# Performance work log

Hardware: AMD Instinct MI355X
Metric: run time of the kernel (lower is better)

Reference implementation:

```python
import jax, jax.numpy as jnp
import numpy as np

FP, DP, K, S, B, T, H, ZD = 96, 28, 3, 4, 64, 8, 512, 2
CP = FP - DP + 1          # 69, valid cross-correlation output size
NP = CP * CP              # 4761 = num_pixels


def setup_inputs() -> dict:
    key = jax.random.key(0)
    ks = jax.random.split(key, 12)
    def rn(k, shape, s=0.02):
        return jax.random.normal(k, shape, jnp.float32) * s
    return {
        "frames": jax.random.uniform(ks[0], (S, B, T, FP, FP), jnp.float32),
        "conv_kernel": jax.random.uniform(ks[1], (S, B, K, DP, DP), jnp.float32),
        "eps": jax.random.normal(ks[2], (S, B, K, ZD), jnp.float32),
        "W1": rn(ks[3], (NP, H)), "b1": jnp.zeros((H,), jnp.float32),
        "Wm1": rn(ks[4], (H, H // 2)), "bm1": jnp.zeros((H // 2,), jnp.float32),
        "Wm2": rn(ks[5], (H // 2, ZD)), "bm2": jnp.zeros((ZD,), jnp.float32),
        "Ws1": rn(ks[6], (H, H // 2)), "bs1": jnp.zeros((H // 2,), jnp.float32),
        "Ws2": rn(ks[7], (H // 2, ZD)), "bs2": jnp.zeros((ZD,), jnp.float32),
        "timestep": 0,
    }


def _axis_weights(p, n):
    """Bilinear 1-D gather indices/weights with zero padding outside [0, n)."""
    p0 = jnp.floor(p)
    f = p - p0
    i0 = p0.astype(jnp.int32)
    i1 = i0 + 1
    w0 = jnp.where((i0 >= 0) & (i0 < n), 1.0 - f, 0.0)
    w1 = jnp.where((i1 >= 0) & (i1 < n), f, 0.0)
    return jnp.clip(i0, 0, n - 1), jnp.clip(i1, 0, n - 1), w0, w1


def _place_digit(digit, zw):
    """AT.digit_to_frame: place DPxDP digit into FPxFP frame at z_where (torch
    affine_grid/grid_sample, align_corners=False, zero padding). theta scale =
    FP/DP, translation = -z_where*FP/DP, i.e. in_coord = (FP/DP)*(out - zw)."""
    scale = FP / DP
    out_c = (2.0 * jnp.arange(FP, dtype=jnp.float32) + 1.0) / FP - 1.0  # (FP,)
    px = ((scale * (out_c - zw[0]) + 1.0) * DP - 1.0) * 0.5  # x source pix
    py = ((scale * (out_c - zw[1]) + 1.0) * DP - 1.0) * 0.5  # y source pix
    y0, y1, wy0, wy1 = _axis_weights(py, DP)
    x0, x1, wx0, wx1 = _axis_weights(px, DP)
    # separable bilinear: interp rows then cols
    tmp = wy0[:, None] * digit[y0, :] + wy1[:, None] * digit[y1, :]  # (FP,DP)
    return wx0[None, :] * tmp[:, x0] + wx1[None, :] * tmp[:, x1]     # (FP,FP)

_place_batch = jax.vmap(_place_digit)


def reference(frames, conv_kernel, eps, W1, b1, Wm1, bm1, Wm2, bm2,
              Ws1, bs1, Ws2, bs2, timestep):
    SB = S * B
    frame_left = frames[:, :, timestep]  # (S,B,FP,FP)
    means, stds, zs = [], [], []
    for k in range(K):
        # per-sample dynamic-kernel cross-correlation via grouped conv
        lhs = frame_left.reshape(1, SB, FP, FP)
        rhs = conv_kernel[:, :, k].reshape(SB, 1, DP, DP)
        conved = jax.lax.conv_general_dilated(
            lhs, rhs, (1, 1), 'VALID', feature_group_count=SB)  # (1,SB,CP,CP)
        scores = jax.nn.softmax(conved.reshape(S, B, NP), axis=-1)
        h = jax.nn.relu(scores @ W1 + b1)                       # (S,B,H)
        mean_k = jnp.tanh(jax.nn.relu(h @ Wm1 + bm1) @ Wm2 + bm2)
        std_k = jnp.exp(jax.nn.relu(h @ Ws1 + bs1) @ Ws2 + bs2)
        z_k = mean_k + std_k * eps[:, :, k]                     # rsample
        recon = _place_batch(conv_kernel[:, :, k].reshape(SB, DP, DP),
                             z_k.reshape(SB, ZD)).reshape(S, B, FP, FP)
        frame_left = frame_left - recon
        means.append(mean_k); stds.append(std_k); zs.append(z_k)
    q_mean = jnp.stack(means, 2)    # (S,B,K,2)
    q_std = jnp.stack(stds, 2)
    z_where = jnp.stack(zs, 2)
    return jnp.stack([q_mean, q_std, z_where], 0)  # (3,S,B,K,2)
```

## Files before the change

### kernel.cpp

```cpp
#include <hip/hip_runtime.h>
#include <hip/hip_bf16.h>
#include <math.h>

#define FPD 96
#define DPD 28
#define CPD 69
#define NPD 4761
#define KKC 3
#define SBN 256
#define TT 8
#define HD 512
#define ZDD 2
#define KPAD 4768
#define SPLITK 15
#define FRS 100

typedef __attribute__((ext_vector_type(8))) short bf16x8;
typedef __attribute__((ext_vector_type(4))) float f32x4;

__device__ __forceinline__ float bf2f(ushort u) {
    union { unsigned int i; float f; } v; v.i = ((unsigned int)u) << 16; return v.f;
}

__global__ __launch_bounds__(256) void w1t_kernel(
    const float* __restrict__ W1, ushort* __restrict__ W1T)
{
    __shared__ ushort tile[64][65];
    const int k0 = blockIdx.x * 64;
    const int n0 = blockIdx.y * 64;
    const int t = threadIdx.x;
    const int ln = t & 63;
    const int lr = t >> 6;

    #pragma unroll
    for (int i = 0; i < 16; ++i) {
        int kk = k0 + lr + i * 4;
        float v = (kk < NPD) ? W1[(size_t)kk * HD + n0 + ln] : 0.f;
        __hip_bfloat16 h = __float2bfloat16(v);
        tile[lr + i * 4][ln] = *reinterpret_cast<ushort*>(&h);
    }
    __syncthreads();
    #pragma unroll
    for (int i = 0; i < 16; ++i) {
        int nn = lr + i * 4;
        int kk = k0 + ln;
        if (kk < KPAD)
            W1T[(size_t)(n0 + nn) * KPAD + kk] = tile[ln][nn];
    }
}

__global__ __launch_bounds__(256) void whid_kernel(
    const float* __restrict__ Wm1, const float* __restrict__ Ws1,
    ushort* __restrict__ Whid)
{
    int i = blockIdx.x * 256 + threadIdx.x;
    const float* src = (i >= 131072) ? Ws1 : Wm1;
    float v = src[i & 131071];
    __hip_bfloat16 h = __float2bfloat16(v);
    Whid[i] = *reinterpret_cast<ushort*>(&h);
}

__global__ __launch_bounds__(1024) void conv_softmax_kernel(
    const float* __restrict__ frames, const int* __restrict__ tsp,
    float* __restrict__ frameL, const float* __restrict__ ck,
    const float* __restrict__ z_cur,
    ushort* __restrict__ e_buf, float* __restrict__ inv_denom, int k)
{
    __shared__ __align__(16) float fr[96 * FRS];
    __shared__ __align__(16) float kr[784];
    __shared__ float dg[784];
    __shared__ float cv[4][NPD];
    __shared__ float red[32];

    const int t = threadIdx.x;
    const int ib = blockIdx.x;

    if (t < 784) {
        kr[t] = ck[((size_t)ib * KKC + k) * 784 + t];
        if (k > 0) dg[t] = ck[((size_t)ib * KKC + (k - 1)) * 784 + t];
    }
    float zx = 0.f, zy = 0.f;
    if (k > 0) { zx = z_cur[ib * 2]; zy = z_cur[ib * 2 + 1]; }
    __syncthreads();

    const float* src = (k < 2)
        ? frames + ((size_t)ib * TT + *tsp) * 9216
        : frameL + (size_t)ib * 9216;
    const float scale = 96.f / 28.f;
    for (int p = t; p < 9216; p += 1024) {
        int r = p / 96, c = p - r * 96;
        float val = src[p];
        if (k > 0) {
            float oci = (2.f * r + 1.f) / 96.f - 1.f;
            float ocj = (2.f * c + 1.f) / 96.f - 1.f;
            float py = ((scale * (oci - zy) + 1.f) * 28.f - 1.f) * 0.5f;
            float px = ((scale * (ocj - zx) + 1.f) * 28.f - 1.f) * 0.5f;
            float py0f = floorf(py), px0f = floorf(px);
            float fy = py - py0f, fx = px - px0f;
            int y0 = (int)py0f, x0 = (int)px0f;
            int y1 = y0 + 1, x1 = x0 + 1;
            float wy0 = (y0 >= 0 && y0 < DPD) ? 1.f - fy : 0.f;
            float wy1 = (y1 >= 0 && y1 < DPD) ? fy : 0.f;
            float wx0 = (x0 >= 0 && x0 < DPD) ? 1.f - fx : 0.f;
            float wx1 = (x1 >= 0 && x1 < DPD) ? fx : 0.f;
            int y0c = min(max(y0, 0), DPD - 1), y1c = min(max(y1, 0), DPD - 1);
            int x0c = min(max(x0, 0), DPD - 1), x1c = min(max(x1, 0), DPD - 1);
            float tmp0 = wy0 * dg[y0c * DPD + x0c] + wy1 * dg[y1c * DPD + x0c];
            float tmp1 = wy0 * dg[y0c * DPD + x1c] + wy1 * dg[y1c * DPD + x1c];
            val -= wx0 * tmp0 + wx1 * tmp1;
        }
        fr[r * FRS + c] = val;
        if (k == 1) frameL[(size_t)ib * 9216 + p] = val;
    }
    if (t < 384) fr[(t >> 2) * FRS + 96 + (t & 3)] = 0.f;
    __syncthreads();

    if (t < 828) {
        const int q    = t / 207;
        const int rem  = t - q * 207;
        const int oy   = rem / 3;
        const int tile = rem - oy * 3;
        const int ox0  = tile * 24;
        const int dy0  = q * 7;

        float acc[24];
        #pragma unroll
        for (int j = 0; j < 24; ++j) acc[j] = 0.f;

        for (int dd = 0; dd < 7; ++dd) {
            const int dy = dy0 + dd;
            const float* frow = &fr[(oy + dy) * FRS + ox0];
            const float* krow = &kr[dy * 28];
            float w[28];
            #pragma unroll
            for (int u = 0; u < 7; ++u) {
                float4 v = *(const float4*)(frow + 4 * u);
                w[4*u] = v.x; w[4*u+1] = v.y; w[4*u+2] = v.z; w[4*u+3] = v.w;
            }
            #pragma unroll
            for (int d = 0; d < 28; d += 4) {
                float4 kv = *(const float4*)(krow + d);
                float kk4[4] = {kv.x, kv.y, kv.z, kv.w};
                #pragma unroll
                for (int i = 0; i < 4; ++i)
                    #pragma unroll
                    for (int j = 0; j < 24; ++j)
                        acc[j] = fmaf(w[i + j], kk4[i], acc[j]);
                if (d < 24) {
                    #pragma unroll
                    for (int qq = 0; qq < 24; ++qq) w[qq] = w[qq + 4];
                    float4 nv = *(const float4*)(frow + d + 28);
                    w[24] = nv.x; w[25] = nv.y; w[26] = nv.z; w[27] = nv.w;
                }
            }
        }
        float* cvq = &cv[q][oy * CPD + ox0];
        #pragma unroll
        for (int j = 0; j < 24; ++j)
            if (ox0 + j < CPD) cvq[j] = acc[j];
    }
    __syncthreads();

    float m = -INFINITY;
    for (int i = t; i < NPD; i += 1024) {
        float v = cv[0][i] + cv[1][i] + cv[2][i] + cv[3][i];
        cv[0][i] = v;
        m = fmaxf(m, v);
    }
    #pragma unroll
    for (int off = 32; off > 0; off >>= 1) m = fmaxf(m, __shfl_down(m, off, 64));
    int lane = t & 63, wid = t >> 6;
    if (lane == 0) red[wid] = m;
    __syncthreads();
    m = red[0];
    #pragma unroll
    for (int i = 1; i < 16; ++i) m = fmaxf(m, red[i]);

    float s = 0.f;
    ushort* eo = e_buf + (size_t)ib * KPAD;
    for (int i = t; i < NPD; i += 1024) {
        float ev = __expf(cv[0][i] - m);
        __hip_bfloat16 h = __float2bfloat16(ev);
        eo[i] = *reinterpret_cast<ushort*>(&h);
        s += ev;
    }
    #pragma unroll
    for (int off = 32; off > 0; off >>= 1) s += __shfl_down(s, off, 64);
    if (lane == 0) red[16 + wid] = s;
    __syncthreads();
    if (t == 0) {
        float tot = 0.f;
        #pragma unroll
        for (int i = 0; i < 16; ++i) tot += red[16 + i];
        inv_denom[ib] = 1.0f / tot;
    }
    if (t < KPAD - NPD) eo[NPD + t] = 0;
}

__global__ __launch_bounds__(256) void gemm1_mfma(
    const ushort* __restrict__ E, const ushort* __restrict__ W1T,
    float* __restrict__ h_acc)
{
    __shared__ __align__(16) ushort As[64][56];
    __shared__ __align__(16) ushort Bs[64][56];

    const int t  = threadIdx.x;
    const int m0 = blockIdx.x * 64;
    const int n0 = blockIdx.y * 64;
    const int z  = blockIdx.z;
    const int step0 = z * 10;
    const int nstep = min(10, 149 - step0);

    const int r = t >> 2;
    const int c = t & 3;
    const int l = t & 63;
    const int w = t >> 6;
    const int lm = l & 15;
    const int kb = l >> 4;

    f32x4 zero = {0.f, 0.f, 0.f, 0.f};
    f32x4 acc[4] = {zero, zero, zero, zero};

    const ushort* eA = E   + (size_t)(m0 + r) * KPAD + c * 8;
    const ushort* eB = W1T + (size_t)(n0 + r) * KPAD + c * 8;

    int k0 = step0 * 32;
    float4 av = *(const float4*)(eA + k0);
    float4 bv = *(const float4*)(eB + k0);

    for (int s = 0; s < nstep; ++s) {
        *(float4*)&As[r][c * 8] = av;
        *(float4*)&Bs[r][c * 8] = bv;
        __syncthreads();
        if (s + 1 < nstep) {
            int kn = (step0 + s + 1) * 32;
            av = *(const float4*)(eA + kn);
            bv = *(const float4*)(eB + kn);
        }
        bf16x8 a = *(const bf16x8*)&As[w * 16 + lm][kb * 8];
        #pragma unroll
        for (int j = 0; j < 4; ++j) {
            bf16x8 b = *(const bf16x8*)&Bs[j * 16 + lm][kb * 8];
            acc[j] = __builtin_amdgcn_mfma_f32_16x16x32_bf16(a, b, acc[j], 0, 0, 0);
        }
        __syncthreads();
    }

    const int mrow = m0 + w * 16 + kb * 4;
    #pragma unroll
    for (int j = 0; j < 4; ++j) {
        int n = n0 + j * 16 + lm;
        #pragma unroll
        for (int rg = 0; rg < 4; ++rg)
            atomicAdd(&h_acc[(size_t)(mrow + rg) * HD + n], acc[j][rg]);
    }
}

__global__ __launch_bounds__(512) void mlp_fused(
    const float* __restrict__ h_acc, const float* __restrict__ inv_denom,
    const float* __restrict__ b1, const ushort* __restrict__ Whid,
    const float* __restrict__ bm1, const float* __restrict__ bs1,
    const float* __restrict__ Wm2, const float* __restrict__ bm2,
    const float* __restrict__ Ws2, const float* __restrict__ bs2,
    const float* __restrict__ eps, float* __restrict__ out,
    float* __restrict__ z_cur, int k)
{
    __shared__ float hsh[2][HD];
    __shared__ float h2[2][2][256];
    __shared__ float res_sh[2][2][2];

    const int t = threadIdx.x;
    const int ib0 = blockIdx.x * 2;

    #pragma unroll
    for (int q = 0; q < 2; ++q) {
        int ib = ib0 + q;
        hsh[q][t] = fmaxf(fmaf(h_acc[(size_t)ib * HD + t], inv_denom[ib], b1[t]), 0.f);
    }
    __syncthreads();

    {
        int head = t >> 8, col = t & 255;
        const ushort* W = Whid + (size_t)head * 131072 + col;
        float bias = head ? bs1[col] : bm1[col];
        float a0 = 0.f, a1 = 0.f;
        #pragma unroll 8
        for (int i = 0; i < HD; ++i) {
            float wf = bf2f(W[(size_t)i * 256]);
            a0 = fmaf(hsh[0][i], wf, a0);
            a1 = fmaf(hsh[1][i], wf, a1);
        }
        h2[head][0][col] = fmaxf(a0 + bias, 0.f);
        h2[head][1][col] = fmaxf(a1 + bias, 0.f);
    }
    __syncthreads();

    {
        int w = t >> 6, l = t & 63;
        int img = w >> 2, zd = (w >> 1) & 1, head = w & 1;
        const float* W2 = head ? Ws2 : Wm2;
        float a = 0.f;
        #pragma unroll
        for (int u = 0; u < 4; ++u) {
            int i = l + u * 64;
            a = fmaf(h2[head][img][i], W2[i * 2 + zd], a);
        }
        #pragma unroll
        for (int off = 32; off > 0; off >>= 1) a += __shfl_down(a, off, 64);
        if (l == 0) {
            float r = head ? __expf(a + bs2[zd]) : tanhf(a + bm2[zd]);
            res_sh[img][zd][head] = r;
        }
    }
    __syncthreads();
    if (t < 4) {
        int img = t >> 1, zd = t & 1, ib = ib0 + img;
        float mean = res_sh[img][zd][0];
        float stdv = res_sh[img][zd][1];
        float ev = eps[(size_t)ib * 6 + k * 2 + zd];
        float z = fmaf(stdv, ev, mean);
        int oidx = ib * 6 + k * 2 + zd;
        out[oidx]        = mean;
        out[1536 + oidx] = stdv;
        out[3072 + oidx] = z;
        z_cur[ib * 2 + zd] = z;
    }
}

extern "C" void kernel_launch(void* const* d_in, const int* in_sizes, int n_in,
                              void* d_out, int out_size, void* d_ws, size_t ws_size,
                              hipStream_t stream)
{
    const float* frames = (const float*)d_in[0];
    const float* ck     = (const float*)d_in[1];
    const float* eps    = (const float*)d_in[2];
    const float* W1     = (const float*)d_in[3];
    const float* b1     = (const float*)d_in[4];
    const float* Wm1    = (const float*)d_in[5];
    const float* bm1    = (const float*)d_in[6];
    const float* Wm2    = (const float*)d_in[7];
    const float* bm2    = (const float*)d_in[8];
    const float* Ws1    = (const float*)d_in[9];
    const float* bs1    = (const float*)d_in[10];
    const float* Ws2    = (const float*)d_in[11];
    const float* bs2    = (const float*)d_in[12];
    const int*   tsp    = (const int*)d_in[13];
    float* out = (float*)d_out;

    float* frameL  = (float*)d_ws;
    float* h_acc   = frameL + 2359296;
    float* inv_den = h_acc + 131072;
    float* z_cur   = inv_den + 256;
    ushort* e_buf  = (ushort*)(z_cur + 512);
    ushort* W1T    = e_buf + (size_t)SBN * KPAD;
    ushort* Whid   = W1T + (size_t)HD * KPAD;

    w1t_kernel<<<dim3(75, 8), 256, 0, stream>>>(W1, W1T);
    whid_kernel<<<1024, 256, 0, stream>>>(Wm1, Ws1, Whid);

    for (int k = 0; k < KKC; ++k) {
        hipMemsetAsync(h_acc, 0, (size_t)SBN * HD * sizeof(float), stream);
        conv_softmax_kernel<<<256, 1024, 0, stream>>>(
            frames, tsp, frameL, ck, z_cur, e_buf, inv_den, k);
        gemm1_mfma<<<dim3(4, 8, SPLITK), 256, 0, stream>>>(e_buf, W1T, h_acc);
        mlp_fused<<<128, 512, 0, stream>>>(h_acc, inv_den, b1, Whid,
                                           bm1, bs1, Wm2, bm2, Ws2, bs2,
                                           eps, out, z_cur, k);
    }
}
```

Before: 345.7 us.

## Replace split-K atomics with partial buffers, transpose hidden weights, restructure conv inner loop

The GEMM now writes per-split partial sums to a workspace buffer instead of using atomicAdd, which also removes the per-step memset; the MLP kernel reduces the 15 partials itself. Hidden-layer weights are pre-transposed so each thread reads contiguous 16-byte bf16 vectors, and the MLP now runs one image per block across 256 blocks. The convolution loads a wider register window so it no longer shifts registers inside the loop, and stores results as float4 into a padded conv buffer. These changes trade extra register pressure and partial-buffer traffic for fewer atomics and better-coalesced loads.

```diff
diff --git a/kernel.cpp b/kernel.cpp
--- a/kernel.cpp
+++ b/kernel.cpp
@@ -14,10 +14,17 @@
 #define KPAD 4768
 #define SPLITK 15
 #define FRS 100
+#define CVS 72
 
 typedef __attribute__((ext_vector_type(8))) short bf16x8;
 typedef __attribute__((ext_vector_type(4))) float f32x4;
 
+__device__ __forceinline__ float bf2f_lo(unsigned int u) {
+    union { unsigned int i; float f; } v; v.i = u << 16; return v.f;
+}
+__device__ __forceinline__ float bf2f_hi(unsigned int u) {
+    union { unsigned int i; float f; } v; v.i = u & 0xffff0000u; return v.f;
+}
 __device__ __forceinline__ float bf2f(ushort u) {
     union { unsigned int i; float f; } v; v.i = ((unsigned int)u) << 16; return v.f;
 }
@@ -49,15 +56,32 @@
     }
 }
 
-__global__ __launch_bounds__(256) void whid_kernel(
+__global__ __launch_bounds__(256) void whidt_kernel(
     const float* __restrict__ Wm1, const float* __restrict__ Ws1,
-    ushort* __restrict__ Whid)
-{
-    int i = blockIdx.x * 256 + threadIdx.x;
-    const float* src = (i >= 131072) ? Ws1 : Wm1;
-    float v = src[i & 131071];
-    __hip_bfloat16 h = __float2bfloat16(v);
-    Whid[i] = *reinterpret_cast<ushort*>(&h);
+    ushort* __restrict__ WhidT)
+{
+    __shared__ ushort tile[64][65];
+    const int i0 = blockIdx.x * 64;
+    const int r0 = blockIdx.y * 64;
+    const int t = threadIdx.x;
+    const int ln = t & 63;
+    const int lr = t >> 6;
+
+    #pragma unroll
+    for (int rep = 0; rep < 16; ++rep) {
+        int i = i0 + lr + rep * 4;
+        int r = r0 + ln;
+        const float* src = (r >= 256) ? Ws1 : Wm1;
+        float v = src[(size_t)i * 256 + (r & 255)];
+        __hip_bfloat16 h = __float2bfloat16(v);
+        tile[lr + rep * 4][ln] = *reinterpret_cast<ushort*>(&h);
+    }
+    __syncthreads();
+    #pragma unroll
+    for (int rep = 0; rep < 16; ++rep) {
+        int r = r0 + lr + rep * 4;
+        WhidT[(size_t)r * 512 + i0 + ln] = tile[ln][lr + rep * 4];
+    }
 }
 
 __global__ __launch_bounds__(1024) void conv_softmax_kernel(
@@ -69,7 +93,7 @@
     __shared__ __align__(16) float fr[96 * FRS];
     __shared__ __align__(16) float kr[784];
     __shared__ float dg[784];
-    __shared__ float cv[4][NPD];
+    __shared__ __align__(16) float cv[4][69 * CVS];
     __shared__ float red[32];
 
     const int t = threadIdx.x;
@@ -127,45 +151,46 @@
         #pragma unroll
         for (int j = 0; j < 24; ++j) acc[j] = 0.f;
 
+        #pragma unroll 1
         for (int dd = 0; dd < 7; ++dd) {
             const int dy = dy0 + dd;
             const float* frow = &fr[(oy + dy) * FRS + ox0];
             const float* krow = &kr[dy * 28];
-            float w[28];
+            float w[52];
             #pragma unroll
-            for (int u = 0; u < 7; ++u) {
+            for (int u = 0; u < 13; ++u) {
                 float4 v = *(const float4*)(frow + 4 * u);
                 w[4*u] = v.x; w[4*u+1] = v.y; w[4*u+2] = v.z; w[4*u+3] = v.w;
             }
             #pragma unroll
             for (int d = 0; d < 28; d += 4) {
                 float4 kv = *(const float4*)(krow + d);
-                float kk4[4] = {kv.x, kv.y, kv.z, kv.w};
                 #pragma unroll
-                for (int i = 0; i < 4; ++i)
-                    #pragma unroll
-                    for (int j = 0; j < 24; ++j)
-                        acc[j] = fmaf(w[i + j], kk4[i], acc[j]);
-                if (d < 24) {
-                    #pragma unroll
-                    for (int qq = 0; qq < 24; ++qq) w[qq] = w[qq + 4];
-                    float4 nv = *(const float4*)(frow + d + 28);
-                    w[24] = nv.x; w[25] = nv.y; w[26] = nv.z; w[27] = nv.w;
+                for (int j = 0; j < 24; ++j) {
+                    acc[j] = fmaf(w[d + j],     kv.x, acc[j]);
+                    acc[j] = fmaf(w[d + j + 1], kv.y, acc[j]);
+                    acc[j] = fmaf(w[d + j + 2], kv.z, acc[j]);
+                    acc[j] = fmaf(w[d + j + 3], kv.w, acc[j]);
                 }
             }
         }
-        float* cvq = &cv[q][oy * CPD + ox0];
-        #pragma unroll
-        for (int j = 0; j < 24; ++j)
-            if (ox0 + j < CPD) cvq[j] = acc[j];
+        float* cvq = &cv[q][oy * CVS + ox0];
+        #pragma unroll
+        for (int u = 0; u < 6; ++u) {
+            float4 v = make_float4(acc[4*u], acc[4*u+1], acc[4*u+2], acc[4*u+3]);
+            *(float4*)(cvq + 4 * u) = v;
+        }
     }
     __syncthreads();
 
     float m = -INFINITY;
-    for (int i = t; i < NPD; i += 1024) {
-        float v = cv[0][i] + cv[1][i] + cv[2][i] + cv[3][i];
-        cv[0][i] = v;
-        m = fmaxf(m, v);
+    for (int p = t; p < 69 * CVS; p += 1024) {
+        int ox = p - (p / CVS) * CVS;
+        if (ox < CPD) {
+            float v = cv[0][p] + cv[1][p] + cv[2][p] + cv[3][p];
+            cv[0][p] = v;
+            m = fmaxf(m, v);
+        }
     }
     #pragma unroll
     for (int off = 32; off > 0; off >>= 1) m = fmaxf(m, __shfl_down(m, off, 64));
@@ -178,11 +203,15 @@
 
     float s = 0.f;
     ushort* eo = e_buf + (size_t)ib * KPAD;
-    for (int i = t; i < NPD; i += 1024) {
-        float ev = __expf(cv[0][i] - m);
-        __hip_bfloat16 h = __float2bfloat16(ev);
-        eo[i] = *reinterpret_cast<ushort*>(&h);
-        s += ev;
+    for (int p = t; p < 69 * CVS; p += 1024) {
+        int oy = p / CVS;
+        int ox = p - oy * CVS;
+        if (ox < CPD) {
+            float ev = __expf(cv[0][p] - m);
+            __hip_bfloat16 h = __float2bfloat16(ev);
+            eo[oy * CPD + ox] = *reinterpret_cast<ushort*>(&h);
+            s += ev;
+        }
     }
     #pragma unroll
     for (int off = 32; off > 0; off >>= 1) s += __shfl_down(s, off, 64);
@@ -199,7 +228,7 @@
 
 __global__ __launch_bounds__(256) void gemm1_mfma(
     const ushort* __restrict__ E, const ushort* __restrict__ W1T,
-    float* __restrict__ h_acc)
+    float* __restrict__ Cpart)
 {
     __shared__ __align__(16) ushort As[64][56];
     __shared__ __align__(16) ushort Bs[64][56];
@@ -252,71 +281,81 @@
         int n = n0 + j * 16 + lm;
         #pragma unroll
         for (int rg = 0; rg < 4; ++rg)
-            atomicAdd(&h_acc[(size_t)(mrow + rg) * HD + n], acc[j][rg]);
+            Cpart[((size_t)z * SBN + mrow + rg) * HD + n] = acc[j][rg];
     }
 }
 
 __global__ __launch_bounds__(512) void mlp_fused(
-    const float* __restrict__ h_acc, const float* __restrict__ inv_denom,
-    const float* __restrict__ b1, const ushort* __restrict__ Whid,
+    const float* __restrict__ Cpart, const float* __restrict__ inv_denom,
+    const float* __restrict__ b1, const ushort* __restrict__ WhidT,
     const float* __restrict__ bm1, const float* __restrict__ bs1,
     const float* __restrict__ Wm2, const float* __restrict__ bm2,
     const float* __restrict__ Ws2, const float* __restrict__ bs2,
     const float* __restrict__ eps, float* __restrict__ out,
     float* __restrict__ z_cur, int k)
 {
-    __shared__ float hsh[2][HD];
-    __shared__ float h2[2][2][256];
-    __shared__ float res_sh[2][2][2];
+    __shared__ float hsh[HD];
+    __shared__ float h2[2][256];
+    __shared__ float res_sh[2][2];
 
     const int t = threadIdx.x;
-    const int ib0 = blockIdx.x * 2;
-
-    #pragma unroll
-    for (int q = 0; q < 2; ++q) {
-        int ib = ib0 + q;
-        hsh[q][t] = fmaxf(fmaf(h_acc[(size_t)ib * HD + t], inv_denom[ib], b1[t]), 0.f);
+    const int ib = blockIdx.x;
+
+    {
+        float s = 0.f;
+        #pragma unroll
+        for (int z = 0; z < SPLITK; ++z)
+            s += Cpart[((size_t)z * SBN + ib) * HD + t];
+        hsh[t] = fmaxf(fmaf(s, inv_denom[ib], b1[t]), 0.f);
     }
     __syncthreads();
 
     {
         int head = t >> 8, col = t & 255;
-        const ushort* W = Whid + (size_t)head * 131072 + col;
+        const uint4* Wr = (const uint4*)(WhidT + (size_t)(head * 256 + col) * 512);
         float bias = head ? bs1[col] : bm1[col];
-        float a0 = 0.f, a1 = 0.f;
+        float a = 0.f;
         #pragma unroll 8
-        for (int i = 0; i < HD; ++i) {
-            float wf = bf2f(W[(size_t)i * 256]);
-            a0 = fmaf(hsh[0][i], wf, a0);
-            a1 = fmaf(hsh[1][i], wf, a1);
-        }
-        h2[head][0][col] = fmaxf(a0 + bias, 0.f);
-        h2[head][1][col] = fmaxf(a1 + bias, 0.f);
+        for (int u = 0; u < 64; ++u) {
+            uint4 wv = Wr[u];
+            const float* hp = &hsh[u * 8];
+            a = fmaf(hp[0], bf2f_lo(wv.x), a);
+            a = fmaf(hp[1], bf2f_hi(wv.x), a);
+            a = fmaf(hp[2], bf2f_lo(wv.y), a);
+            a = fmaf(hp[3], bf2f_hi(wv.y), a);
+            a = fmaf(hp[4], bf2f_lo(wv.z), a);
+            a = fmaf(hp[5], bf2f_hi(wv.z), a);
+            a = fmaf(hp[6], bf2f_lo(wv.w), a);
+            a = fmaf(hp[7], bf2f_hi(wv.w), a);
+        }
+        h2[head][col] = fmaxf(a + bias, 0.f);
     }
     __syncthreads();
 
     {
         int w = t >> 6, l = t & 63;
-        int img = w >> 2, zd = (w >> 1) & 1, head = w & 1;
-        const float* W2 = head ? Ws2 : Wm2;
-        float a = 0.f;
-        #pragma unroll
-        for (int u = 0; u < 4; ++u) {
-            int i = l + u * 64;
-            a = fmaf(h2[head][img][i], W2[i * 2 + zd], a);
-        }
-        #pragma unroll
-        for (int off = 32; off > 0; off >>= 1) a += __shfl_down(a, off, 64);
-        if (l == 0) {
-            float r = head ? __expf(a + bs2[zd]) : tanhf(a + bm2[zd]);
-            res_sh[img][zd][head] = r;
-        }
-    }
-    __syncthreads();
-    if (t < 4) {
-        int img = t >> 1, zd = t & 1, ib = ib0 + img;
-        float mean = res_sh[img][zd][0];
-        float stdv = res_sh[img][zd][1];
+        if (w < 4) {
+            int zd = (w >> 1) & 1, head = w & 1;
+            const float* W2 = head ? Ws2 : Wm2;
+            float a = 0.f;
+            #pragma unroll
+            for (int u = 0; u < 4; ++u) {
+                int i = l + u * 64;
+                a = fmaf(h2[head][i], W2[i * 2 + zd], a);
+            }
+            #pragma unroll
+            for (int off = 32; off > 0; off >>= 1) a += __shfl_down(a, off, 64);
+            if (l == 0) {
+                float r = head ? __expf(a + bs2[zd]) : tanhf(a + bm2[zd]);
+                res_sh[zd][head] = r;
+            }
+        }
+    }
+    __syncthreads();
+    if (t < 2) {
+        int zd = t;
+        float mean = res_sh[zd][0];
+        float stdv = res_sh[zd][1];
         float ev = eps[(size_t)ib * 6 + k * 2 + zd];
         float z = fmaf(stdv, ev, mean);
         int oidx = ib * 6 + k * 2 + zd;
@@ -348,22 +387,21 @@
     float* out = (float*)d_out;
 
     float* frameL  = (float*)d_ws;
-    float* h_acc   = frameL + 2359296;
-    float* inv_den = h_acc + 131072;
+    float* Cpart   = frameL + 2359296;
+    float* inv_den = Cpart + 1966080;
     float* z_cur   = inv_den + 256;
     ushort* e_buf  = (ushort*)(z_cur + 512);
     ushort* W1T    = e_buf + (size_t)SBN * KPAD;
-    ushort* Whid   = W1T + (size_t)HD * KPAD;
+    ushort* WhidT  = W1T + (size_t)HD * KPAD;
 
     w1t_kernel<<<dim3(75, 8), 256, 0, stream>>>(W1, W1T);
-    whid_kernel<<<1024, 256, 0, stream>>>(Wm1, Ws1, Whid);
+    whidt_kernel<<<dim3(8, 8), 256, 0, stream>>>(Wm1, Ws1, WhidT);
 
     for (int k = 0; k < KKC; ++k) {
-        hipMemsetAsync(h_acc, 0, (size_t)SBN * HD * sizeof(float), stream);
         conv_softmax_kernel<<<256, 1024, 0, stream>>>(
             frames, tsp, frameL, ck, z_cur, e_buf, inv_den, k);
-        gemm1_mfma<<<dim3(4, 8, SPLITK), 256, 0, stream>>>(e_buf, W1T, h_acc);
-        mlp_fused<<<128, 512, 0, stream>>>(h_acc, inv_den, b1, Whid,
+        gemm1_mfma<<<dim3(4, 8, SPLITK), 256, 0, stream>>>(e_buf, W1T, Cpart);
+        mlp_fused<<<256, 512, 0, stream>>>(Cpart, inv_den, b1, WhidT,
                                            bm1, bs1, Wm2, bm2, Ws2, bs2,
                                            eps, out, z_cur, k);
     }
```

Result: faster. 315.6 us (-8.7%).
